# Kernel tuning notes

Hardware: AMD Instinct MI355X
Metric: run time of the kernel (lower is better)

Reference implementation:

```python
import jax, jax.numpy as jnp
import numpy as np

EPS = 1e-5

def _conv1x1(x, w):
    # w: [out_ch, in_ch], x: [n, c, h, w] -> [n, out_ch, h, w]
    return jnp.einsum('oc,nchw->nohw', w, x)

def _bn_relu(x, g, b, m, v):
    # inference-mode BatchNorm2d followed by ReLU
    s = g * jax.lax.rsqrt(v + EPS)
    return jax.nn.relu(x * s[None, :, None, None] + (b - m * s)[None, :, None, None])

def setup_inputs() -> dict:
    N, C, H, W, Kc, K = 8, 512, 128, 128, 512, 19
    keys = iter(jax.random.split(jax.random.key(0), 64))
    d = {}
    d['x'] = jax.random.normal(next(keys), (N, C, H, W), jnp.float32)
    d['proxy'] = jax.random.normal(next(keys), (N, C, K, 1), jnp.float32)
    for nm, shp in [('wp1', (Kc, C)), ('wp2', (Kc, Kc)), ('wo1', (Kc, C)),
                    ('wo2', (Kc, Kc)), ('wd', (Kc, C)), ('wu', (C, Kc))]:
        d[nm] = jax.random.normal(next(keys), shp, jnp.float32) * np.float32(1.0 / np.sqrt(shp[1]))
    for tag, ch in [('p1', Kc), ('p2', Kc), ('o1', Kc), ('o2', Kc), ('d', Kc), ('u', C)]:
        d['g' + tag] = 1.0 + 0.1 * jax.random.normal(next(keys), (ch,), jnp.float32)
        d['b' + tag] = 0.1 * jax.random.normal(next(keys), (ch,), jnp.float32)
        d['m' + tag] = 0.1 * jax.random.normal(next(keys), (ch,), jnp.float32)
        d['v' + tag] = jax.random.uniform(next(keys), (ch,), jnp.float32, 0.5, 1.5)
    return d

def reference(x, proxy,
              wp1, gp1, bp1, mp1, vp1, wp2, gp2, bp2, mp2, vp2,
              wo1, go1, bo1, mo1, vo1, wo2, go2, bo2, mo2, vo2,
              wd, gd, bd, md, vd, wu, gu, bu, mu, vu):
    # scale == 1: no pooling / upsampling
    # f_pixel: two 1x1 conv + BN + ReLU on pixel features
    q = _bn_relu(_conv1x1(x, wp1), gp1, bp1, mp1, vp1)
    q = _bn_relu(_conv1x1(q, wp2), gp2, bp2, mp2, vp2)        # [n, kc, h, w]
    n, kc, h, w = q.shape
    q = q.reshape(n, kc, h * w)                               # [n, kc, hw]
    # f_object on proxy (object region representations)
    k = _bn_relu(_conv1x1(proxy, wo1), go1, bo1, mo1, vo1)
    k = _bn_relu(_conv1x1(k, wo2), go2, bo2, mo2, vo2).reshape(n, kc, -1)  # [n, kc, K]
    # f_down (value)
    v = _bn_relu(_conv1x1(proxy, wd), gd, bd, md, vd).reshape(n, kc, -1)   # [n, kc, K]
    # cross-attention: pixels attend over object regions
    sim = jnp.einsum('ncq,nck->nqk', q, k) * (kc ** -0.5)     # [n, hw, K]
    attn = jax.nn.softmax(sim, axis=-1)
    ctx = jnp.einsum('nqk,nck->ncq', attn, v).reshape(n, kc, h, w)
    # f_up: 1x1 conv + BN + ReLU back to in_channels
    return _bn_relu(_conv1x1(ctx, wu), gu, bu, mu, vu)
```

## Files before the change

kernel.cpp:

```cpp
#include <hip/hip_runtime.h>
#include <stdint.h>

#define HW 16384
#define CH 512
#define KR 19

typedef float f32x4 __attribute__((ext_vector_type(4)));
typedef _Float16 half8 __attribute__((ext_vector_type(8)));
typedef unsigned short us8 __attribute__((ext_vector_type(8)));
typedef unsigned short us4 __attribute__((ext_vector_type(4)));

__device__ __forceinline__ unsigned short f2h(float f) {
    union { _Float16 h; unsigned short u; } v; v.h = (_Float16)f; return v.u;
}
__device__ __forceinline__ float h2f(unsigned short u) {
    union { unsigned short u; _Float16 h; } v; v.u = u; return (float)v.h;
}

__global__ void ObjectAttentionBlock_1176821039805_kernel() {}

__global__ __launch_bounds__(256) void prep_kernel(
    const float* __restrict__ wp1, const float* __restrict__ wp2, const float* __restrict__ wu,
    unsigned short* __restrict__ wp1h, unsigned short* __restrict__ wp2h, unsigned short* __restrict__ wuh,
    const float* gp1, const float* bp1, const float* mp1, const float* vp1,
    const float* gp2, const float* bp2, const float* mp2, const float* vp2,
    const float* gu,  const float* bu,  const float* mu,  const float* vu,
    float* __restrict__ cons)
{
    int i = blockIdx.x * 256 + threadIdx.x;
    if (i < CH * CH) {
        wp1h[i] = f2h(wp1[i]);
        wp2h[i] = f2h(wp2[i]);
        wuh[i]  = f2h(wu[i]);
    }
    if (i < CH) {
        float s1 = gp1[i] * rsqrtf(vp1[i] + 1e-5f);
        cons[i] = s1;          cons[512 + i]  = bp1[i] - mp1[i] * s1;
        float s2 = gp2[i] * rsqrtf(vp2[i] + 1e-5f);
        cons[1024 + i] = s2;   cons[1536 + i] = bp2[i] - mp2[i] * s2;
        float su = gu[i] * rsqrtf(vu[i] + 1e-5f);
        cons[2048 + i] = su;   cons[2560 + i] = bu[i] - mu[i] * su;
    }
}

__global__ __launch_bounds__(256) void transpose_kernel(
    const float* __restrict__ x, unsigned short* __restrict__ xT)
{
    __shared__ unsigned short t[64][66];
    const int n  = blockIdx.z;
    const int c0 = blockIdx.y * 64;
    const int m0 = blockIdx.x * 64;
    const int tx = threadIdx.x & 63;
    const int ty = threadIdx.x >> 6;
    const float* xb = x + ((size_t)n * CH + c0) * HW + m0;
    #pragma unroll
    for (int r = 0; r < 16; ++r) {
        int cl = ty * 16 + r;
        t[cl][tx] = f2h(xb[(size_t)cl * HW + tx]);
    }
    __syncthreads();
    unsigned short* xo = xT + ((size_t)n * HW + m0) * CH + c0;
    #pragma unroll
    for (int r = 0; r < 16; ++r) {
        int ml = ty * 16 + r;
        xo[(size_t)ml * CH + tx] = t[tx][ml];
    }
}

__global__ __launch_bounds__(256) void kv1_kernel(
    const float* __restrict__ proxy, const float* __restrict__ wo1, const float* __restrict__ wd,
    const float* go1, const float* bo1, const float* mo1, const float* vo1,
    const float* gd,  const float* bd,  const float* md,  const float* vd,
    float* __restrict__ t1, float* __restrict__ vout)
{
    const int n  = blockIdx.x;
    const int o0 = blockIdx.y * 64;
    const float* px = proxy + (size_t)n * CH * KR;
    for (int idx = threadIdx.x; idx < 64 * KR; idx += 256) {
        int o = o0 + idx / KR;
        int j = idx % KR;
        float a1 = 0.f, a2 = 0.f;
        for (int c = 0; c < CH; ++c) {
            float p = px[c * KR + j];
            a1 += wo1[o * CH + c] * p;
            a2 += wd [o * CH + c] * p;
        }
        float s1 = go1[o] * rsqrtf(vo1[o] + 1e-5f);
        float s2 = gd[o]  * rsqrtf(vd[o]  + 1e-5f);
        t1  [((size_t)n * CH + o) * KR + j] = fmaxf(a1 * s1 + (bo1[o] - mo1[o] * s1), 0.f);
        vout[((size_t)n * CH + o) * KR + j] = fmaxf(a2 * s2 + (bd[o]  - md[o]  * s2), 0.f);
    }
}

__global__ __launch_bounds__(256) void kv2_kernel(
    const float* __restrict__ t1, const float* __restrict__ wo2,
    const float* go2, const float* bo2, const float* mo2, const float* vo2,
    float* __restrict__ kout)
{
    const int n  = blockIdx.x;
    const int o0 = blockIdx.y * 64;
    const float* tb = t1 + (size_t)n * CH * KR;
    for (int idx = threadIdx.x; idx < 64 * KR; idx += 256) {
        int o = o0 + idx / KR;
        int j = idx % KR;
        float a = 0.f;
        for (int c = 0; c < CH; ++c) a += wo2[o * CH + c] * tb[c * KR + j];
        float s = go2[o] * rsqrtf(vo2[o] + 1e-5f);
        kout[((size_t)n * CH + o) * KR + j] = fmaxf(a * s + (bo2[o] - mo2[o] * s), 0.f);
    }
}

__global__ __launch_bounds__(256) void pad_kernel(
    const float* __restrict__ kbuf, const float* __restrict__ vbuf,
    unsigned short* __restrict__ kt, unsigned short* __restrict__ vt)
{
    int idx = blockIdx.x * 256 + threadIdx.x;
    int n = idx >> 16, rem = idx & 65535;
    int j = rem >> 9, c = rem & 511;
    kt[idx] = (j < KR) ? f2h(kbuf[((size_t)(n * CH + c)) * KR + j]) : (unsigned short)0;
    int c2 = rem >> 7, j2 = rem & 127;
    vt[idx] = (j2 < KR) ? f2h(vbuf[((size_t)(n * CH + c2)) * KR + j2]) : (unsigned short)0;
}

template<int MODE, int BN>
__global__ __launch_bounds__(256) void gemm_nt(
    const unsigned short* __restrict__ A,
    const unsigned short* __restrict__ W,
    const float* __restrict__ sc, const float* __restrict__ sh,
    void* __restrict__ outp)
{
    __shared__ __align__(16) char lds_raw[64 * 132 * 4];
    unsigned short* stage = (unsigned short*)lds_raw;
    float (*epi)[132] = (float (*)[132])lds_raw;

    const int tid  = threadIdx.x;
    const int lane = tid & 63;
    const int wm = (tid >> 7) & 1;
    const int wn = (tid >> 6) & 1;
    const int id  = blockIdx.x;
    const int swz = (id & 7) * 512 + (id >> 3);
    const int i0 = (swz >> 2) << 7;
    const int j0 = (swz & 3) << 7;

    size_t gA[4], gW[4];
    int ldso[4];
    #pragma unroll
    for (int q = 0; q < 4; ++q) {
        int ca = q * 256 + tid;
        int r = ca >> 3, p = ca & 7;
        gA[q] = (size_t)(i0 + r) * 512 + p * 8;
        gW[q] = (size_t)(j0 + r) * 512 + p * 8;
        ldso[q] = r * 64 + ((p ^ (r & 7)) << 3);
    }

    us8 va[4], vb[4];
    #pragma unroll
    for (int q = 0; q < 4; ++q) {
        va[q] = *(const us8*)(A + gA[q]);
        vb[q] = *(const us8*)(W + gW[q]);
    }

    f32x4 acc[4][4];
    #pragma unroll
    for (int i = 0; i < 4; ++i)
        #pragma unroll
        for (int j = 0; j < 4; ++j) acc[i][j] = (f32x4){0.f, 0.f, 0.f, 0.f};

    const int arow = wm * 64 + (lane & 15);
    const int brow = wn * 64 + (lane & 15);
    const int kch  = lane >> 4;

    for (int kk = 0; kk < 8; ++kk) {
        __syncthreads();
        #pragma unroll
        for (int q = 0; q < 4; ++q) {
            *(us8*)(stage + ldso[q]) = va[q];
            *(us8*)(stage + 8192 + ldso[q]) = vb[q];
        }
        __syncthreads();
        if (kk < 7) {
            #pragma unroll
            for (int q = 0; q < 4; ++q) {
                va[q] = *(const us8*)(A + gA[q] + (kk + 1) * 64);
                vb[q] = *(const us8*)(W + gW[q] + (kk + 1) * 64);
            }
        }
        #pragma unroll
        for (int s = 0; s < 2; ++s) {
            half8 af[4], bw[4];
            #pragma unroll
            for (int t = 0; t < 4; ++t) {
                int ra = arow + t * 16;
                af[t] = *(const half8*)(stage + ra * 64 + (((s * 4 + kch) ^ (ra & 7)) << 3));
                int rb = brow + t * 16;
                bw[t] = *(const half8*)(stage + 8192 + rb * 64 + (((s * 4 + kch) ^ (rb & 7)) << 3));
            }
            #pragma unroll
            for (int i = 0; i < 4; ++i)
                #pragma unroll
                for (int j = 0; j < 4; ++j)
                    acc[i][j] = __builtin_amdgcn_mfma_f32_16x16x32_f16(af[i], bw[j], acc[i][j], 0, 0, 0);
        }
    }

    float scv[4], shv[4];
    #pragma unroll
    for (int j = 0; j < 4; ++j) {
        int gj = j0 + wn * 64 + j * 16 + (lane & 15);
        scv[j] = BN ? sc[gj] : 1.0f;
        shv[j] = BN ? sh[gj] : 0.0f;
    }

    if (MODE == 0) {
        unsigned short* op = (unsigned short*)outp;
        #pragma unroll
        for (int i = 0; i < 4; ++i) {
            int gi = i0 + wm * 64 + i * 16 + (lane >> 4) * 4;
            #pragma unroll
            for (int j = 0; j < 4; ++j) {
                int gj = j0 + wn * 64 + j * 16 + (lane & 15);
                #pragma unroll
                for (int r = 0; r < 4; ++r) {
                    float vv = acc[i][j][r];
                    if (BN) vv = fmaxf(vv * scv[j] + shv[j], 0.f);
                    op[(size_t)(gi + r) * 512 + gj] = f2h(vv);
                }
            }
        }
    } else {
        float* op = (float*)outp;
        const int n  = i0 >> 14;
        const int mb = i0 & (HW - 1);
        #pragma unroll
        for (int h = 0; h < 2; ++h) {
            __syncthreads();
            if (wn == h) {
                #pragma unroll
                for (int j = 0; j < 4; ++j) {
                    int ljh = j * 16 + (lane & 15);
                    #pragma unroll
                    for (int i = 0; i < 4; ++i) {
                        int li = wm * 64 + i * 16 + (lane >> 4) * 4;
                        f32x4 vv;
                        #pragma unroll
                        for (int r = 0; r < 4; ++r)
                            vv[r] = fmaxf(acc[i][j][r] * scv[j] + shv[j], 0.f);
                        *(f32x4*)&epi[ljh][li] = vv;
                    }
                }
            }
            __syncthreads();
            #pragma unroll
            for (int q = 0; q < 8; ++q) {
                int idx = q * 256 + tid;
                int ch = idx >> 5, chunk = idx & 31;
                f32x4 v = *(const f32x4*)&epi[ch][chunk * 4];
                size_t base = ((size_t)(n * 512 + j0 + h * 64 + ch) << 14) + mb + chunk * 4;
                op[base] = v[0]; op[base + 1] = v[1]; op[base + 2] = v[2]; op[base + 3] = v[3];
            }
        }
    }
}

__global__ __launch_bounds__(256) void attn_fused(
    const unsigned short* __restrict__ q2,
    const unsigned short* __restrict__ ktg,
    const unsigned short* __restrict__ vtg,
    unsigned short* __restrict__ ctx)
{
    __shared__ __align__(16) char lds[47104];
    unsigned short* stage = (unsigned short*)lds;
    unsigned short* vt_l  = (unsigned short*)lds;
    unsigned short* att_l = (unsigned short*)(lds + 36864);

    const int tid  = threadIdx.x;
    const int lane = tid & 63;
    const int w    = tid >> 6;
    const int i0   = blockIdx.x * 128;
    const int n    = blockIdx.x >> 7;
    const unsigned short* KT = ktg + n * 65536;
    const unsigned short* VT = vtg + n * 65536;

    size_t gA[4]; int loA[4];
    #pragma unroll
    for (int q = 0; q < 4; ++q) {
        int ca = q * 256 + tid;
        int r = ca >> 3, p = ca & 7;
        gA[q] = (size_t)(i0 + r) * 512 + p * 8;
        loA[q] = r * 64 + ((p ^ (r & 7)) << 3);
    }
    const int rB = tid >> 3, pB = tid & 7;
    const size_t gB = (size_t)rB * 512 + pB * 8;
    const int loB = 8192 + rB * 64 + ((pB ^ (rB & 7)) << 3);

    us8 va[4], vbk;
    #pragma unroll
    for (int q = 0; q < 4; ++q) va[q] = *(const us8*)(q2 + gA[q]);
    vbk = *(const us8*)(KT + gB);

    f32x4 acc[2][2];
    #pragma unroll
    for (int i = 0; i < 2; ++i)
        #pragma unroll
        for (int j = 0; j < 2; ++j) acc[i][j] = (f32x4){0.f, 0.f, 0.f, 0.f};

    const int kch = lane >> 4;
    for (int kk = 0; kk < 8; ++kk) {
        __syncthreads();
        #pragma unroll
        for (int q = 0; q < 4; ++q) *(us8*)(stage + loA[q]) = va[q];
        *(us8*)(stage + loB) = vbk;
        __syncthreads();
        if (kk < 7) {
            #pragma unroll
            for (int q = 0; q < 4; ++q) va[q] = *(const us8*)(q2 + gA[q] + (kk + 1) * 64);
            vbk = *(const us8*)(KT + gB + (kk + 1) * 64);
        }
        #pragma unroll
        for (int s = 0; s < 2; ++s) {
            half8 af[2], bf[2];
            #pragma unroll
            for (int i = 0; i < 2; ++i) {
                int ra = w * 32 + i * 16 + (lane & 15);
                af[i] = *(const half8*)(stage + ra * 64 + (((s * 4 + kch) ^ (ra & 7)) << 3));
            }
            #pragma unroll
            for (int t = 0; t < 2; ++t) {
                int rb = t * 16 + (lane & 15);
                bf[t] = *(const half8*)(stage + 8192 + rb * 64 + (((s * 4 + kch) ^ (rb & 7)) << 3));
            }
            #pragma unroll
            for (int i = 0; i < 2; ++i)
                #pragma unroll
                for (int j = 0; j < 2; ++j)
                    acc[i][j] = __builtin_amdgcn_mfma_f32_16x16x32_f16(af[i], bf[j], acc[i][j], 0, 0, 0);
        }
    }

    const float scale = 0.044194173824159216f;
    const bool v1 = (lane & 15) < 3;
    unsigned short a16[2][4][2];
    #pragma unroll
    for (int i = 0; i < 2; ++i) {
        #pragma unroll
        for (int r = 0; r < 4; ++r) {
            float s0 = acc[i][0][r] * scale;
            float s1v = acc[i][1][r] * scale;
            float m = v1 ? fmaxf(s0, s1v) : s0;
            m = fmaxf(m, __shfl_xor(m, 1));
            m = fmaxf(m, __shfl_xor(m, 2));
            m = fmaxf(m, __shfl_xor(m, 4));
            m = fmaxf(m, __shfl_xor(m, 8));
            float a0 = __expf(s0 - m);
            float a1 = v1 ? __expf(s1v - m) : 0.f;
            float sm = a0 + a1;
            sm += __shfl_xor(sm, 1);
            sm += __shfl_xor(sm, 2);
            sm += __shfl_xor(sm, 4);
            sm += __shfl_xor(sm, 8);
            float inv = 1.0f / sm;
            a16[i][r][0] = f2h(a0 * inv);
            a16[i][r][1] = f2h(a1 * inv);
        }
    }
    #pragma unroll
    for (int i = 0; i < 2; ++i)
        #pragma unroll
        for (int r = 0; r < 4; ++r) {
            int R = w * 32 + i * 16 + (lane >> 4) * 4 + r;
            att_l[R * 40 + (lane & 15)]      = a16[i][r][0];
            att_l[R * 40 + 16 + (lane & 15)] = a16[i][r][1];
        }
    __syncthreads();

    #pragma unroll
    for (int q = 0; q < 8; ++q) {
        int id = q * 256 + tid;
        int c = id >> 2, part = id & 3;
        us8 v = *(const us8*)(VT + (size_t)c * 128 + part * 8);
        *(us4*)(vt_l + c * 36 + part * 8)     = (us4){v[0], v[1], v[2], v[3]};
        *(us4*)(vt_l + c * 36 + part * 8 + 4) = (us4){v[4], v[5], v[6], v[7]};
    }
    __syncthreads();

    half8 a2[2];
    #pragma unroll
    for (int i = 0; i < 2; ++i) {
        int R = w * 32 + i * 16 + (lane & 15);
        a2[i] = *(const half8*)(att_l + R * 40 + (lane >> 4) * 8);
    }
    #pragma unroll
    for (int jc = 0; jc < 4; ++jc) {
        half8 bf[8];
        #pragma unroll
        for (int t = 0; t < 8; ++t) {
            int c = jc * 128 + t * 16 + (lane & 15);
            const unsigned short* pb = vt_l + c * 36 + (lane >> 4) * 8;
            us4 lo = *(const us4*)(pb);
            us4 hi = *(const us4*)(pb + 4);
            us8 u = {lo[0], lo[1], lo[2], lo[3], hi[0], hi[1], hi[2], hi[3]};
            bf[t] = *(half8*)&u;
        }
        #pragma unroll
        for (int i = 0; i < 2; ++i) {
            #pragma unroll
            for (int t = 0; t < 8; ++t) {
                f32x4 o = __builtin_amdgcn_mfma_f32_16x16x32_f16(
                    a2[i], bf[t], (f32x4){0.f, 0.f, 0.f, 0.f}, 0, 0, 0);
                int col = jc * 128 + t * 16 + (lane & 15);
                int row = i0 + w * 32 + i * 16 + (lane >> 4) * 4;
                #pragma unroll
                for (int r = 0; r < 4; ++r)
                    ctx[(size_t)(row + r) * 512 + col] = f2h(o[r]);
            }
        }
    }
}

extern "C" void kernel_launch(void* const* d_in, const int* in_sizes, int n_in,
                              void* d_out, int out_size, void* d_ws, size_t ws_size,
                              hipStream_t stream)
{
    const float* x     = (const float*)d_in[0];
    const float* proxy = (const float*)d_in[1];
    const float* wp1   = (const float*)d_in[2];
    const float* wp2   = (const float*)d_in[3];
    const float* wo1   = (const float*)d_in[4];
    const float* wo2   = (const float*)d_in[5];
    const float* wd    = (const float*)d_in[6];
    const float* wu    = (const float*)d_in[7];
    const float* gp1 = (const float*)d_in[8],  *bp1 = (const float*)d_in[9];
    const float* mp1 = (const float*)d_in[10], *vp1 = (const float*)d_in[11];
    const float* gp2 = (const float*)d_in[12], *bp2 = (const float*)d_in[13];
    const float* mp2 = (const float*)d_in[14], *vp2 = (const float*)d_in[15];
    const float* go1 = (const float*)d_in[16], *bo1 = (const float*)d_in[17];
    const float* mo1 = (const float*)d_in[18], *vo1 = (const float*)d_in[19];
    const float* go2 = (const float*)d_in[20], *bo2 = (const float*)d_in[21];
    const float* mo2 = (const float*)d_in[22], *vo2 = (const float*)d_in[23];
    const float* gd  = (const float*)d_in[24], *bd  = (const float*)d_in[25];
    const float* md  = (const float*)d_in[26], *vd  = (const float*)d_in[27];
    const float* gu  = (const float*)d_in[28], *bu  = (const float*)d_in[29];
    const float* mu  = (const float*)d_in[30], *vu  = (const float*)d_in[31];

    char* ws = (char*)d_ws;
    unsigned short* r0   = (unsigned short*)ws;
    unsigned short* wp1h = (unsigned short*)(ws + 134217728);
    unsigned short* wp2h = wp1h + 262144;
    unsigned short* wuh  = wp2h + 262144;
    float* t1   = (float*)(wuh + 262144);
    float* kbuf = t1 + 8 * CH * KR;
    float* vbuf = kbuf + 8 * CH * KR;
    float* cons = vbuf + 8 * CH * KR;

    float* outf = (float*)d_out;
    unsigned short* outh = (unsigned short*)d_out;
    unsigned short* q1T = outh;
    unsigned short* ktb = outh + 117440512;
    unsigned short* vtb = outh + 117964800;

    prep_kernel<<<1024, 256, 0, stream>>>(wp1, wp2, wu, wp1h, wp2h, wuh,
        gp1, bp1, mp1, vp1, gp2, bp2, mp2, vp2, gu, bu, mu, vu, cons);
    transpose_kernel<<<dim3(256, 8, 8), 256, 0, stream>>>(x, r0);
    kv1_kernel<<<dim3(8, 8), 256, 0, stream>>>(proxy, wo1, wd,
        go1, bo1, mo1, vo1, gd, bd, md, vd, t1, vbuf);
    kv2_kernel<<<dim3(8, 8), 256, 0, stream>>>(t1, wo2, go2, bo2, mo2, vo2, kbuf);
    pad_kernel<<<2048, 256, 0, stream>>>(kbuf, vbuf, ktb, vtb);

    gemm_nt<0, 1><<<4096, 256, 0, stream>>>(r0, wp1h, cons, cons + 512, q1T);
    gemm_nt<0, 1><<<4096, 256, 0, stream>>>(q1T, wp2h, cons + 1024, cons + 1536, r0);
    attn_fused<<<1024, 256, 0, stream>>>(r0, ktb, vtb, r0);
    gemm_nt<1, 1><<<4096, 256, 0, stream>>>(r0, wuh, cons + 2048, cons + 2560, outf);
}
```

Measured before the change: 735.4 us.

## Rewrite GEMMs as 256x256-tile double-buffered kernels with direct global-to-LDS loads

Replaces the 128x128 register-staged GEMM with a 512-thread, 256x256-tile kernel that uses global_load_lds to copy tiles straight into a double-buffered 128KB LDS region, with explicit vmcnt waits and barriers. Larger tiles raise arithmetic intensity and reuse of A and W, and async prefetch two stages ahead overlaps loads with MFMA. The fp32 epilogue now writes vectorised 16-byte stores. In exchange occupancy drops to one block per CU with heavy register use (128 accumulators per lane), and the grid shrinks to 1024 blocks.

```diff
diff --git a/kernel.cpp b/kernel.cpp
--- a/kernel.cpp
+++ b/kernel.cpp
@@ -15,6 +15,13 @@
 }
 __device__ __forceinline__ float h2f(unsigned short u) {
     union { unsigned short u; _Float16 h; } v; v.u = u; return (float)v.h;
+}
+
+__device__ __forceinline__ void gll16(const void* g, void* l) {
+    __builtin_amdgcn_global_load_lds(
+        (const __attribute__((address_space(1))) unsigned int*)g,
+        (__attribute__((address_space(3))) unsigned int*)l,
+        16, 0, 0);
 }
 
 __global__ void ObjectAttentionBlock_1176821039805_kernel() {}
@@ -123,140 +130,145 @@
 }
 
 template<int MODE, int BN>
-__global__ __launch_bounds__(256) void gemm_nt(
+__global__ __launch_bounds__(512, 1) void gemm256(
     const unsigned short* __restrict__ A,
     const unsigned short* __restrict__ W,
     const float* __restrict__ sc, const float* __restrict__ sh,
     void* __restrict__ outp)
 {
-    __shared__ __align__(16) char lds_raw[64 * 132 * 4];
-    unsigned short* stage = (unsigned short*)lds_raw;
-    float (*epi)[132] = (float (*)[132])lds_raw;
+    __shared__ __align__(16) char lds[131072];
 
     const int tid  = threadIdx.x;
     const int lane = tid & 63;
-    const int wm = (tid >> 7) & 1;
-    const int wn = (tid >> 6) & 1;
-    const int id  = blockIdx.x;
-    const int swz = (id & 7) * 512 + (id >> 3);
-    const int i0 = (swz >> 2) << 7;
-    const int j0 = (swz & 3) << 7;
-
-    size_t gA[4], gW[4];
-    int ldso[4];
-    #pragma unroll
-    for (int q = 0; q < 4; ++q) {
-        int ca = q * 256 + tid;
-        int r = ca >> 3, p = ca & 7;
-        gA[q] = (size_t)(i0 + r) * 512 + p * 8;
-        gW[q] = (size_t)(j0 + r) * 512 + p * 8;
-        ldso[q] = r * 64 + ((p ^ (r & 7)) << 3);
-    }
-
-    us8 va[4], vb[4];
-    #pragma unroll
-    for (int q = 0; q < 4; ++q) {
-        va[q] = *(const us8*)(A + gA[q]);
-        vb[q] = *(const us8*)(W + gW[q]);
-    }
-
-    f32x4 acc[4][4];
-    #pragma unroll
-    for (int i = 0; i < 4; ++i)
+    const int w    = tid >> 6;
+    const int wm   = w >> 2;
+    const int wn   = w & 3;
+    const int id   = blockIdx.x;
+    const int swz  = (id & 7) * 128 + (id >> 3);
+    const int i0   = (swz >> 1) << 8;
+    const int j0   = (swz & 1) << 8;
+
+    const int lr = lane >> 3;
+    const int lc = (lane & 7) ^ (lane >> 3);
+
+    f32x4 acc[8][4];
+    #pragma unroll
+    for (int i = 0; i < 8; ++i)
         #pragma unroll
         for (int j = 0; j < 4; ++j) acc[i][j] = (f32x4){0.f, 0.f, 0.f, 0.f};
 
-    const int arow = wm * 64 + (lane & 15);
-    const int brow = wn * 64 + (lane & 15);
-    const int kch  = lane >> 4;
-
-    for (int kk = 0; kk < 8; ++kk) {
-        __syncthreads();
+    const int rl  = lane & 15;
+    const int kch = lane >> 4;
+
+    auto stage = [&](int t) {
+        char* db = lds + (t & 1) * 65536;
         #pragma unroll
         for (int q = 0; q < 4; ++q) {
-            *(us8*)(stage + ldso[q]) = va[q];
-            *(us8*)(stage + 8192 + ldso[q]) = vb[q];
-        }
-        __syncthreads();
-        if (kk < 7) {
-            #pragma unroll
-            for (int q = 0; q < 4; ++q) {
-                va[q] = *(const us8*)(A + gA[q] + (kk + 1) * 64);
-                vb[q] = *(const us8*)(W + gW[q] + (kk + 1) * 64);
-            }
-        }
+            int grp = q * 8 + w;
+            gll16(A + (size_t)(i0 + grp * 8 + lr) * 512 + t * 64 + lc * 8,
+                  db + q * 8192 + w * 1024);
+        }
+        #pragma unroll
+        for (int q = 0; q < 4; ++q) {
+            int grp = q * 8 + w;
+            gll16(W + (size_t)(j0 + grp * 8 + lr) * 512 + t * 64 + lc * 8,
+                  db + 32768 + q * 8192 + w * 1024);
+        }
+    };
+
+    stage(0);
+    stage(1);
+
+    for (int t = 0; t < 8; ++t) {
+        if (t < 7) asm volatile("s_waitcnt vmcnt(8)" ::: "memory");
+        else       asm volatile("s_waitcnt vmcnt(0)" ::: "memory");
+        __builtin_amdgcn_sched_barrier(0);
+        __builtin_amdgcn_s_barrier();
+        __builtin_amdgcn_sched_barrier(0);
+
+        const unsigned short* db = (const unsigned short*)(lds + (t & 1) * 65536);
+        __builtin_amdgcn_s_setprio(1);
         #pragma unroll
         for (int s = 0; s < 2; ++s) {
-            half8 af[4], bw[4];
-            #pragma unroll
-            for (int t = 0; t < 4; ++t) {
-                int ra = arow + t * 16;
-                af[t] = *(const half8*)(stage + ra * 64 + (((s * 4 + kch) ^ (ra & 7)) << 3));
-                int rb = brow + t * 16;
-                bw[t] = *(const half8*)(stage + 8192 + rb * 64 + (((s * 4 + kch) ^ (rb & 7)) << 3));
-            }
-            #pragma unroll
-            for (int i = 0; i < 4; ++i)
+            half8 af[8], bw[4];
+            #pragma unroll
+            for (int rf = 0; rf < 8; ++rf) {
+                int ra = wm * 128 + rf * 16 + rl;
+                af[rf] = *(const half8*)(db + ra * 64 + (((s * 4 + kch) ^ (ra & 7)) << 3));
+            }
+            #pragma unroll
+            for (int cf = 0; cf < 4; ++cf) {
+                int rb = wn * 64 + cf * 16 + rl;
+                bw[cf] = *(const half8*)(db + 16384 + rb * 64 + (((s * 4 + kch) ^ (rb & 7)) << 3));
+            }
+            #pragma unroll
+            for (int rf = 0; rf < 8; ++rf)
                 #pragma unroll
-                for (int j = 0; j < 4; ++j)
-                    acc[i][j] = __builtin_amdgcn_mfma_f32_16x16x32_f16(af[i], bw[j], acc[i][j], 0, 0, 0);
-        }
+                for (int cf = 0; cf < 4; ++cf)
+                    acc[rf][cf] = __builtin_amdgcn_mfma_f32_16x16x32_f16(af[rf], bw[cf], acc[rf][cf], 0, 0, 0);
+        }
+        __builtin_amdgcn_s_setprio(0);
+        __builtin_amdgcn_sched_barrier(0);
+        __builtin_amdgcn_s_barrier();
+        __builtin_amdgcn_sched_barrier(0);
+        if (t < 6) stage(t + 2);
     }
 
     float scv[4], shv[4];
     #pragma unroll
-    for (int j = 0; j < 4; ++j) {
-        int gj = j0 + wn * 64 + j * 16 + (lane & 15);
-        scv[j] = BN ? sc[gj] : 1.0f;
-        shv[j] = BN ? sh[gj] : 0.0f;
+    for (int cf = 0; cf < 4; ++cf) {
+        int gj = j0 + wn * 64 + cf * 16 + rl;
+        scv[cf] = BN ? sc[gj] : 1.0f;
+        shv[cf] = BN ? sh[gj] : 0.0f;
     }
 
     if (MODE == 0) {
         unsigned short* op = (unsigned short*)outp;
         #pragma unroll
-        for (int i = 0; i < 4; ++i) {
-            int gi = i0 + wm * 64 + i * 16 + (lane >> 4) * 4;
-            #pragma unroll
-            for (int j = 0; j < 4; ++j) {
-                int gj = j0 + wn * 64 + j * 16 + (lane & 15);
+        for (int rf = 0; rf < 8; ++rf) {
+            int gi = i0 + wm * 128 + rf * 16 + (lane >> 4) * 4;
+            #pragma unroll
+            for (int cf = 0; cf < 4; ++cf) {
+                int gj = j0 + wn * 64 + cf * 16 + rl;
                 #pragma unroll
-                for (int r = 0; r < 4; ++r) {
-                    float vv = acc[i][j][r];
-                    if (BN) vv = fmaxf(vv * scv[j] + shv[j], 0.f);
-                    op[(size_t)(gi + r) * 512 + gj] = f2h(vv);
+                for (int e = 0; e < 4; ++e) {
+                    float vv = acc[rf][cf][e];
+                    if (BN) vv = fmaxf(vv * scv[cf] + shv[cf], 0.f);
+                    op[(size_t)(gi + e) * 512 + gj] = f2h(vv);
                 }
             }
         }
     } else {
         float* op = (float*)outp;
+        float (*epi)[260] = (float (*)[260])lds;
         const int n  = i0 >> 14;
         const int mb = i0 & (HW - 1);
-        #pragma unroll
-        for (int h = 0; h < 2; ++h) {
+        const int ch  = tid >> 3;
+        const int prt = tid & 7;
+        #pragma unroll
+        for (int g = 0; g < 4; ++g) {
             __syncthreads();
-            if (wn == h) {
+            if (wn == g) {
                 #pragma unroll
-                for (int j = 0; j < 4; ++j) {
-                    int ljh = j * 16 + (lane & 15);
+                for (int cf = 0; cf < 4; ++cf) {
+                    int chl = cf * 16 + rl;
                     #pragma unroll
-                    for (int i = 0; i < 4; ++i) {
-                        int li = wm * 64 + i * 16 + (lane >> 4) * 4;
+                    for (int rf = 0; rf < 8; ++rf) {
+                        int px = wm * 128 + rf * 16 + (lane >> 4) * 4;
                         f32x4 vv;
                         #pragma unroll
-                        for (int r = 0; r < 4; ++r)
-                            vv[r] = fmaxf(acc[i][j][r] * scv[j] + shv[j], 0.f);
-                        *(f32x4*)&epi[ljh][li] = vv;
+                        for (int e = 0; e < 4; ++e)
+                            vv[e] = fmaxf(acc[rf][cf][e] * scv[cf] + shv[cf], 0.f);
+                        *(f32x4*)&epi[chl][px] = vv;
                     }
                 }
             }
             __syncthreads();
-            #pragma unroll
-            for (int q = 0; q < 8; ++q) {
-                int idx = q * 256 + tid;
-                int ch = idx >> 5, chunk = idx & 31;
-                f32x4 v = *(const f32x4*)&epi[ch][chunk * 4];
-                size_t base = ((size_t)(n * 512 + j0 + h * 64 + ch) << 14) + mb + chunk * 4;
-                op[base] = v[0]; op[base + 1] = v[1]; op[base + 2] = v[2]; op[base + 3] = v[3];
+            size_t base = ((size_t)(n * 512 + j0 + g * 64 + ch) << 14) + mb + prt * 32;
+            #pragma unroll
+            for (int u = 0; u < 8; ++u) {
+                f32x4 v = *(const f32x4*)&epi[ch][prt * 32 + u * 4];
+                *(f32x4*)&op[base + u * 4] = v;
             }
         }
     }
@@ -466,8 +478,8 @@
     kv2_kernel<<<dim3(8, 8), 256, 0, stream>>>(t1, wo2, go2, bo2, mo2, vo2, kbuf);
     pad_kernel<<<2048, 256, 0, stream>>>(kbuf, vbuf, ktb, vtb);
 
-    gemm_nt<0, 1><<<4096, 256, 0, stream>>>(r0, wp1h, cons, cons + 512, q1T);
-    gemm_nt<0, 1><<<4096, 256, 0, stream>>>(q1T, wp2h, cons + 1024, cons + 1536, r0);
+    gemm256<0, 1><<<1024, 512, 0, stream>>>(r0, wp1h, cons, cons + 512, q1T);
+    gemm256<0, 1><<<1024, 512, 0, stream>>>(q1T, wp2h, cons + 1024, cons + 1536, r0);
     attn_fused<<<1024, 256, 0, stream>>>(r0, ktb, vtb, r0);
-    gemm_nt<1, 1><<<4096, 256, 0, stream>>>(r0, wuh, cons + 2048, cons + 2560, outf);
-}
+    gemm256<1, 1><<<1024, 512, 0, stream>>>(r0, wuh, cons + 2048, cons + 2560, outf);
+}
```

Result: faster. 707.8 us (-3.7%).

## Stage GEMM tiles via direct global-to-LDS loads with double buffering

Applied to the files above, without the earlier changes.

Replaces the register-staged global loads and LDS stores in the fp16 MFMA GEMM with global_load_lds direct transfers into a double-buffered 64KB LDS region. The next K-tile is issued before computing on the current one, and one barrier per iteration replaces two. This aims to cut register pressure and VGPR-to-LDS store traffic and to overlap loads with MFMA. The cost is doubled LDS use, which may lower occupancy. Correctness depends on the swizzle layout produced by the direct loads and on wait/barrier ordering.

```diff
diff --git a/kernel.cpp b/kernel.cpp
--- a/kernel.cpp
+++ b/kernel.cpp
@@ -15,6 +15,13 @@
 }
 __device__ __forceinline__ float h2f(unsigned short u) {
     union { unsigned short u; _Float16 h; } v; v.u = u; return (float)v.h;
+}
+
+__device__ __forceinline__ void gll16(const void* g, void* l) {
+    __builtin_amdgcn_global_load_lds(
+        (const __attribute__((address_space(1))) unsigned int*)g,
+        (__attribute__((address_space(3))) unsigned int*)l,
+        16, 0, 0);
 }
 
 __global__ void ObjectAttentionBlock_1176821039805_kernel() {}
@@ -129,12 +136,12 @@
     const float* __restrict__ sc, const float* __restrict__ sh,
     void* __restrict__ outp)
 {
-    __shared__ __align__(16) char lds_raw[64 * 132 * 4];
-    unsigned short* stage = (unsigned short*)lds_raw;
+    __shared__ __align__(16) char lds_raw[65536];
     float (*epi)[132] = (float (*)[132])lds_raw;
 
     const int tid  = threadIdx.x;
     const int lane = tid & 63;
+    const int wave = tid >> 6;
     const int wm = (tid >> 7) & 1;
     const int wn = (tid >> 6) & 1;
     const int id  = blockIdx.x;
@@ -142,23 +149,8 @@
     const int i0 = (swz >> 2) << 7;
     const int j0 = (swz & 3) << 7;
 
-    size_t gA[4], gW[4];
-    int ldso[4];
-    #pragma unroll
-    for (int q = 0; q < 4; ++q) {
-        int ca = q * 256 + tid;
-        int r = ca >> 3, p = ca & 7;
-        gA[q] = (size_t)(i0 + r) * 512 + p * 8;
-        gW[q] = (size_t)(j0 + r) * 512 + p * 8;
-        ldso[q] = r * 64 + ((p ^ (r & 7)) << 3);
-    }
-
-    us8 va[4], vb[4];
-    #pragma unroll
-    for (int q = 0; q < 4; ++q) {
-        va[q] = *(const us8*)(A + gA[q]);
-        vb[q] = *(const us8*)(W + gW[q]);
-    }
+    const int lrow = lane >> 3;
+    const int lsw  = ((lane & 7) ^ (lane >> 3)) * 16;
 
     f32x4 acc[4][4];
     #pragma unroll
@@ -170,30 +162,33 @@
     const int brow = wn * 64 + (lane & 15);
     const int kch  = lane >> 4;
 
-    for (int kk = 0; kk < 8; ++kk) {
-        __syncthreads();
+    auto stageF = [&](int t) {
+        char* db = lds_raw + (t & 1) * 32768;
         #pragma unroll
         for (int q = 0; q < 4; ++q) {
-            *(us8*)(stage + ldso[q]) = va[q];
-            *(us8*)(stage + 8192 + ldso[q]) = vb[q];
-        }
-        __syncthreads();
-        if (kk < 7) {
-            #pragma unroll
-            for (int q = 0; q < 4; ++q) {
-                va[q] = *(const us8*)(A + gA[q] + (kk + 1) * 64);
-                vb[q] = *(const us8*)(W + gW[q] + (kk + 1) * 64);
-            }
-        }
+            int rg = wave * 32 + q * 8;
+            gll16((const char*)A + ((size_t)(i0 + rg + lrow) * 512 + t * 64) * 2 + lsw,
+                  db + rg * 128);
+            gll16((const char*)W + ((size_t)(j0 + rg + lrow) * 512 + t * 64) * 2 + lsw,
+                  db + 16384 + rg * 128);
+        }
+    };
+
+    stageF(0);
+    __syncthreads();
+
+    for (int t = 0; t < 8; ++t) {
+        if (t < 7) stageF(t + 1);
+        const unsigned short* stage = (const unsigned short*)(lds_raw + (t & 1) * 32768);
         #pragma unroll
         for (int s = 0; s < 2; ++s) {
             half8 af[4], bw[4];
             #pragma unroll
-            for (int t = 0; t < 4; ++t) {
-                int ra = arow + t * 16;
-                af[t] = *(const half8*)(stage + ra * 64 + (((s * 4 + kch) ^ (ra & 7)) << 3));
-                int rb = brow + t * 16;
-                bw[t] = *(const half8*)(stage + 8192 + rb * 64 + (((s * 4 + kch) ^ (rb & 7)) << 3));
+            for (int u = 0; u < 4; ++u) {
+                int ra = arow + u * 16;
+                af[u] = *(const half8*)(stage + ra * 64 + (((s * 4 + kch) ^ (ra & 7)) << 3));
+                int rb = brow + u * 16;
+                bw[u] = *(const half8*)(stage + 8192 + rb * 64 + (((s * 4 + kch) ^ (rb & 7)) << 3));
             }
             #pragma unroll
             for (int i = 0; i < 4; ++i)
@@ -201,6 +196,7 @@
                 for (int j = 0; j < 4; ++j)
                     acc[i][j] = __builtin_amdgcn_mfma_f32_16x16x32_f16(af[i], bw[j], acc[i][j], 0, 0, 0);
         }
+        __syncthreads();
     }
 
     float scv[4], shv[4];
```

Result: no change. 725.6 us (-1.3%).
